# Kernel tuning notes

Measured on AMD Instinct MI355X. Metric: run time of the kernel, lower is better.

Reference implementation:

```python
import jax, jax.numpy as jnp
import numpy as np

EPS = 1e-5  # torch BatchNorm2d default eps


def _conv(x, w, b, pad):
    y = jax.lax.conv_general_dilated(
        x, w, window_strides=(1, 1), padding=[(pad, pad), (pad, pad)],
        dimension_numbers=('NCHW', 'OIHW', 'NCHW'))
    return y + b[None, :, None, None]


def _bn_train(x, gamma, beta):
    # training-mode BatchNorm2d: biased batch statistics over (N,H,W)
    m = jnp.mean(x, axis=(0, 2, 3), keepdims=True)
    v = jnp.var(x, axis=(0, 2, 3), keepdims=True)
    xn = (x - m) * jax.lax.rsqrt(v + EPS)
    return xn * gamma[None, :, None, None] + beta[None, :, None, None]


def _ncc(s, t):
    # Vectorized equivalent of the per-pixel double loop.
    # ncc[b,0,i,j] = mean(tt * ss / (tt_std * ss_std)) over (C,th,tw)
    #             = sum(tt * s_sub) / (N * tt_std * ss_std)   (since sum(tt)=0)
    b, c, sh, sw = s.shape
    th, tw = t.shape[2], t.shape[3]
    N = c * th * tw
    tt = t - jnp.mean(t, axis=(1, 2, 3), keepdims=True)
    # torch.std is unbiased (divides by N-1)
    tt_std = jnp.sqrt(jnp.sum(tt * tt, axis=(1, 2, 3), keepdims=True) / (N - 1))

    # cross[b] = valid correlation of s[b] with its own template tt[b]
    def per_sample(si, ti):
        return jax.lax.conv_general_dilated(
            si[None], ti[None], (1, 1), 'VALID',
            dimension_numbers=('NCHW', 'OIHW', 'NCHW'))[0]  # (1,h,w)

    cross = jax.vmap(per_sample)(s, tt)  # (b,1,h,w)

    # per-window mean/std of s via box-filter conv over all C channels jointly
    box = jnp.ones((1, c, th, tw), dtype=s.dtype)
    win_sum = jax.lax.conv_general_dilated(
        s, box, (1, 1), 'VALID', dimension_numbers=('NCHW', 'OIHW', 'NCHW'))
    win_sqsum = jax.lax.conv_general_dilated(
        s * s, box, (1, 1), 'VALID', dimension_numbers=('NCHW', 'OIHW', 'NCHW'))
    win_mean = win_sum / N
    ss_var = jnp.maximum(win_sqsum - N * win_mean * win_mean, 0.0) / (N - 1)
    ss_std = jnp.sqrt(ss_var)

    return cross / (N * tt_std * ss_std)  # (b,1,h,w)


def reference(s, t, w1, b1, g1, be1, w2, b2, g2, be2,
              w3, b3, g3, be3, w4, b4):
    s = _bn_train(_conv(s, w1, b1, pad=1), g1, be1)
    t = _bn_train(_conv(t, w2, b2, pad=1), g2, be2)
    ncc = _ncc(s, t)
    x = _bn_train(_conv(ncc, w3, b3, pad=0), g3, be3)
    x = jax.nn.relu(x)
    return _conv(x, w4, b4, pad=0)  # (b,2,h,w)


def setup_inputs() -> dict:
    key = jax.random.key(0)
    ks = jax.random.split(key, 12)
    C = 256
    inp = {
        's': jax.random.normal(ks[0], (16, C, 64, 64), jnp.float32),
        't': jax.random.normal(ks[1], (16, C, 16, 16), jnp.float32),
        'w1': jax.random.normal(ks[2], (C, C, 3, 3), jnp.float32) * 0.02,
        'b1': jax.random.normal(ks[3], (C,), jnp.float32) * 0.02,
        'g1': jnp.ones((C,), jnp.float32),
        'be1': jnp.zeros((C,), jnp.float32),
        'w2': jax.random.normal(ks[4], (C, C, 3, 3), jnp.float32) * 0.02,
        'b2': jax.random.normal(ks[5], (C,), jnp.float32) * 0.02,
        'g2': jnp.ones((C,), jnp.float32),
        'be2': jnp.zeros((C,), jnp.float32),
        'w3': jax.random.normal(ks[6], (1, 1, 1, 1), jnp.float32),
        'b3': jax.random.normal(ks[7], (1,), jnp.float32) * 0.02,
        'g3': jnp.ones((1,), jnp.float32),
        'be3': jnp.zeros((1,), jnp.float32),
        'w4': jax.random.normal(ks[8], (2, 1, 1, 1), jnp.float32),
        'b4': jax.random.normal(ks[9], (2,), jnp.float32) * 0.02,
    }
    return inp
```

## Files before the change

kernel.cpp:

```cpp
#include <hip/hip_runtime.h>
#include <hip/hip_bf16.h>

#define EPSV 1e-5f

constexpr int B_ = 16, C_ = 256;
constexpr int OHW_ = 49 * 49;
constexpr int NTOT = 256 * 16 * 16;
constexpr int GROUPS = 32, CPERG = 8;

typedef short bf16x8 __attribute__((ext_vector_type(8)));
typedef float f32x4 __attribute__((ext_vector_type(4)));

constexpr size_t OFF_S1 = 0;
constexpr size_t SZ_S1  = (size_t)16 * 256 * 4096;
constexpr size_t OFF_T2 = OFF_S1 + SZ_S1;
constexpr size_t SZ_T2  = (size_t)16 * 256 * 256;
constexpr size_t OFF_ST = OFF_T2 + SZ_T2;
constexpr size_t OFF_C  = OFF_ST + 2048;
constexpr size_t SPC_BYTES = (size_t)16 * 66 * 66 * 256 * 2;
constexpr size_t TPC_BYTES = (size_t)16 * 18 * 18 * 256 * 2;
constexpr size_t WR_BYTES  = (size_t)9 * 256 * 256 * 2;
constexpr size_t ZOFF  = 0;
constexpr size_t CPOFF = 131072;
constexpr size_t NCOFF = CPOFF + (size_t)GROUPS * 16 * OHW_;
constexpr size_t SATOFF = NCOFF + (size_t)16 * OHW_;

__device__ __forceinline__ void gload_lds16(const void* g, void* l) {
    __builtin_amdgcn_global_load_lds((const __attribute__((address_space(1))) unsigned int*)g,
                                     (__attribute__((address_space(3))) unsigned int*)l,
                                     16, 0, 0);
}

template<int W>
__global__ __launch_bounds__(256)
void pad_transpose(const float* __restrict__ in, __hip_bfloat16* __restrict__ outp)
{
    constexpr int PW = W + 2;
    __shared__ float tile[64][W + 1];
    int bid = blockIdx.x;
    int icg = bid & 3; bid >>= 2;
    int yp = bid % PW; bid /= PW;
    int b = bid;
    int ic0 = icg * 64;
    int tid = threadIdx.x;
    bool interior = (yp >= 1 && yp <= W);
    if (interior) {
        int y = yp - 1;
        for (int idx = tid; idx < 64 * W; idx += 256) {
            int i = idx / W, x = idx % W;
            tile[i][x] = in[(((size_t)(b * C_ + ic0 + i)) * W + y) * W + x];
        }
    }
    __syncthreads();
    for (int idx = tid; idx < PW * 16; idx += 256) {
        int xp = idx >> 4, i4 = idx & 15;
        ushort4 v = make_ushort4(0, 0, 0, 0);
        if (interior && xp >= 1 && xp <= W) {
            #pragma unroll
            for (int k = 0; k < 4; ++k) {
                __hip_bfloat16 h = __float2bfloat16(tile[i4 * 4 + k][xp - 1]);
                reinterpret_cast<unsigned short*>(&v)[k] = *reinterpret_cast<unsigned short*>(&h);
            }
        }
        *reinterpret_cast<ushort4*>(&outp[(((size_t)(b * PW) + yp) * PW + xp) * 256 + ic0 + i4 * 4]) = v;
    }
}

__global__ __launch_bounds__(256)
void weight_reorg(const float* __restrict__ w, __hip_bfloat16* __restrict__ wr)
{
    int idx = blockIdx.x * 256 + threadIdx.x;
    const float* src = w + (size_t)idx * 9;
    #pragma unroll
    for (int t = 0; t < 9; ++t)
        wr[(size_t)t * 65536 + idx] = __float2bfloat16(src[t]);
}

template<int W>
__global__ __launch_bounds__(256)
void conv_mfma(const __hip_bfloat16* __restrict__ SPc, const __hip_bfloat16* __restrict__ Wr,
               const float* __restrict__ bias, float* __restrict__ out,
               float* __restrict__ csum, float* __restrict__ csq)
{
    constexpr int PW = W + 2;
    constexpr int NPIX = W * W;
    constexpr int NT = NPIX / 128;
    __shared__ __hip_bfloat16 A_lds[128 * 32];
    __shared__ __hip_bfloat16 B_lds[128 * 32];

    int bid = blockIdx.x;
    int nt = bid % NT; bid /= NT;
    int mt = bid & 1;  bid >>= 1;
    int b  = bid;
    int tid = threadIdx.x;
    int lane = tid & 63;
    int wv = tid >> 6, wm = wv >> 1, wn = wv & 1;
    int oc0 = mt * 128, p0 = nt * 128;

    f32x4 acc[4][4];
    #pragma unroll
    for (int i = 0; i < 4; ++i)
        #pragma unroll
        for (int j = 0; j < 4; ++j)
            #pragma unroll
            for (int r = 0; r < 4; ++r) acc[i][j][r] = 0.f;

    const bf16x8* Af = reinterpret_cast<const bf16x8*>(A_lds);
    const bf16x8* Bf = reinterpret_cast<const bf16x8*>(B_lds);
    int colb = lane >> 4;
    int rA = lane & 15;

    for (int kc = 0; kc < 72; ++kc) {
        int tap = kc >> 3, icc = kc & 7;
        int ic0 = icc * 32;
        int dy = tap / 3, dx = tap - dy * 3;
        __syncthreads();
        #pragma unroll
        for (int it = 0; it < 2; ++it) {
            int sIdx = tid + it * 256;
            int row = sIdx >> 2, seg = sIdx & 3;
            const __hip_bfloat16* srcA =
                Wr + ((size_t)(tap * 256 + oc0 + row)) * 256 + ic0 + seg * 8;
            gload_lds16(srcA, &A_lds[sIdx * 8]);
            int p = p0 + row;
            int y = p / W, x = p % W;
            const __hip_bfloat16* srcB =
                SPc + (((size_t)(b * PW + y + dy)) * PW + x + dx) * 256 + ic0 + seg * 8;
            gload_lds16(srcB, &B_lds[sIdx * 8]);
        }
        asm volatile("s_waitcnt vmcnt(0)" ::: "memory");
        __syncthreads();

        bf16x8 a[4], bb[4];
        #pragma unroll
        for (int mi = 0; mi < 4; ++mi)
            a[mi] = Af[(wm * 64 + mi * 16 + rA) * 4 + colb];
        #pragma unroll
        for (int ni = 0; ni < 4; ++ni)
            bb[ni] = Bf[(wn * 64 + ni * 16 + rA) * 4 + colb];
        #pragma unroll
        for (int mi = 0; mi < 4; ++mi)
            #pragma unroll
            for (int ni = 0; ni < 4; ++ni)
                acc[mi][ni] = __builtin_amdgcn_mfma_f32_16x16x32_bf16(
                    a[mi], bb[ni], acc[mi][ni], 0, 0, 0);
    }

    #pragma unroll
    for (int mi = 0; mi < 4; ++mi) {
        int ocb = oc0 + wm * 64 + mi * 16 + (lane >> 4) * 4;
        #pragma unroll
        for (int r = 0; r < 4; ++r) {
            int oc = ocb + r;
            float bv = bias[oc];
            float* orow = out + ((size_t)(b * C_ + oc)) * NPIX;
            float s_oc = 0.f, q_oc = 0.f;
            #pragma unroll
            for (int ni = 0; ni < 4; ++ni) {
                int px = p0 + wn * 64 + ni * 16 + (lane & 15);
                float v = acc[mi][ni][r] + bv;
                orow[px] = v;
                s_oc += v; q_oc += v * v;
            }
            #pragma unroll
            for (int m_ = 1; m_ < 16; m_ <<= 1) {
                s_oc += __shfl_xor(s_oc, m_);
                q_oc += __shfl_xor(q_oc, m_);
            }
            if ((lane & 15) == 0) {
                atomicAdd(&csum[oc], s_oc);
                atomicAdd(&csq[oc], q_oc);
            }
        }
    }
}

__device__ inline void blk_reduce2(float& a, float& q, int tid) {
    #pragma unroll
    for (int off = 32; off > 0; off >>= 1) {
        a += __shfl_down(a, off);
        q += __shfl_down(q, off);
    }
    __shared__ float ra[4], rq[4];
    if ((tid & 63) == 0) { ra[tid >> 6] = a; rq[tid >> 6] = q; }
    __syncthreads();
    if (tid == 0) { a = ra[0] + ra[1] + ra[2] + ra[3]; q = rq[0] + rq[1] + rq[2] + rq[3]; }
}

__global__ __launch_bounds__(256)
void bn_norm(float* __restrict__ x, const float* __restrict__ csum,
             const float* __restrict__ csq, const float* __restrict__ g,
             const float* __restrict__ be, int HW, int total4, float inv_cnt)
{
    int i = blockIdx.x * 256 + threadIdx.x;
    if (i >= total4) return;
    int c = ((i * 4) / HW) % C_;
    float m = csum[c] * inv_cnt;
    float v = csq[c] * inv_cnt - m * m;
    float sc = rsqrtf(v + EPSV) * g[c];
    float sh = be[c] - m * sc;
    float4 val = reinterpret_cast<float4*>(x)[i];
    val.x = val.x * sc + sh;
    val.y = val.y * sc + sh;
    val.z = val.z * sc + sh;
    val.w = val.w * sc + sh;
    reinterpret_cast<float4*>(x)[i] = val;
}

__global__ __launch_bounds__(256)
void zplane_kernel(const float* __restrict__ s1, const float* __restrict__ csum,
                   const float* __restrict__ csq, const float* __restrict__ g1,
                   const float* __restrict__ be1, float* __restrict__ z)
{
    __shared__ float SC[256], SH[256];
    int tid = threadIdx.x;
    {
        float m = csum[tid] * (1.f / 65536.f);
        float v = csq[tid] * (1.f / 65536.f) - m * m;
        float sc = rsqrtf(v + EPSV) * g1[tid];
        SC[tid] = sc; SH[tid] = be1[tid] - m * sc;
    }
    __syncthreads();
    int i = blockIdx.x * 256 + tid;
    int b = i >> 12, p = i & 4095;
    const float* base = s1 + (size_t)b * (C_ * 4096) + p;
    float s = 0.f, q = 0.f;
    for (int c = 0; c < C_; ++c) {
        float val = base[(size_t)c * 4096] * SC[c] + SH[c];
        s += val; q += val * val;
    }
    z[i] = s; z[65536 + i] = q;
}

__global__ __launch_bounds__(256)
void sat_kernel(const float* __restrict__ zin, float* __restrict__ sat)
{
    __shared__ float t[65][66];
    int pl = blockIdx.x;
    int tid = threadIdx.x;
    const float* src = zin + (size_t)pl * 4096;
    for (int idx = tid; idx < 4096; idx += 256) {
        int y = idx >> 6, x = idx & 63;
        t[y + 1][x + 1] = src[idx];
    }
    for (int idx = tid; idx < 65; idx += 256) { t[0][idx] = 0.f; t[idx][0] = 0.f; }
    __syncthreads();
    if (tid < 64) {
        float run = 0.f;
        for (int x = 1; x <= 64; ++x) { run += t[tid + 1][x]; t[tid + 1][x] = run; }
    }
    __syncthreads();
    if (tid < 64) {
        float run = 0.f;
        for (int y = 1; y <= 64; ++y) { run += t[y][tid + 1]; t[y][tid + 1] = run; }
    }
    __syncthreads();
    float* dst = sat + (size_t)pl * 4225;
    for (int idx = tid; idx < 4225; idx += 256) {
        int r = idx / 65, c = idx % 65;
        dst[idx] = t[r][c];
    }
}

__global__ __launch_bounds__(256)
void tstat_kernel(const float* __restrict__ t2, float* __restrict__ tmean, float* __restrict__ ttstd)
{
    int b = blockIdx.x, tid = threadIdx.x;
    const float* p = t2 + (size_t)b * NTOT;
    float s = 0.f, q = 0.f;
    for (int i = tid; i < NTOT; i += 256) { float v = p[i]; s += v; q += v * v; }
    blk_reduce2(s, q, tid);
    if (tid == 0) {
        float m = s / (float)NTOT;
        tmean[b] = m;
        ttstd[b] = sqrtf(fmaxf(q - (float)NTOT * m * m, 0.f) / (float)(NTOT - 1));
    }
}

__global__ __launch_bounds__(256, 2)
void cross_v3(const float* __restrict__ s1, const float* __restrict__ t2,
              const float* __restrict__ csum, const float* __restrict__ csq,
              const float* __restrict__ g1, const float* __restrict__ be1,
              float* __restrict__ cpart)
{
    __shared__ float4 spl4[1024];
    __shared__ float tpl[256];
    __shared__ float red[4][64][49];

    int g = blockIdx.x & (GROUPS - 1);
    int b = blockIdx.x / GROUPS;
    int tid = threadIdx.x;
    int phase = tid >> 6;
    int lane = tid & 63;
    int i = lane;
    int i_ld = i < 49 ? i : 48;

    float acc[49];
    #pragma unroll
    for (int j = 0; j < 49; ++j) acc[j] = 0.f;

    #pragma unroll 1
    for (int cc = 0; cc < CPERG; ++cc) {
        int c = g * CPERG + cc;
        float m = csum[c] * (1.f / 65536.f);
        float v = csq[c] * (1.f / 65536.f) - m * m;
        float sc = rsqrtf(v + EPSV) * g1[c];
        float sh = be1[c] - m * sc;
        __syncthreads();
        const float4* sp4 = reinterpret_cast<const float4*>(s1 + ((size_t)(b * C_ + c)) * 4096);
        #pragma unroll
        for (int k = 0; k < 4; ++k) {
            int gidx = tid + k * 256;
            float4 val = sp4[gidx];
            val.x = val.x * sc + sh; val.y = val.y * sc + sh;
            val.z = val.z * sc + sh; val.w = val.w * sc + sh;
            int row = gidx >> 4, jg = gidx & 15;
            spl4[row * 16 + (jg ^ (row & 7))] = val;
        }
        tpl[tid] = t2[((size_t)(b * C_ + c)) * 256 + tid];
        __syncthreads();
        #pragma unroll 1
        for (int tyl = 0; tyl < 4; ++tyl) {
            int ty = phase * 4 + tyl;
            int row = i_ld + ty;
            float r_[64];
            #pragma unroll
            for (int jg = 0; jg < 16; ++jg) {
                float4 v4 = spl4[row * 16 + (jg ^ (row & 7))];
                r_[jg * 4 + 0] = v4.x; r_[jg * 4 + 1] = v4.y;
                r_[jg * 4 + 2] = v4.z; r_[jg * 4 + 3] = v4.w;
            }
            float tt[16];
            const float4* tp4 = reinterpret_cast<const float4*>(&tpl[ty * 16]);
            #pragma unroll
            for (int k = 0; k < 4; ++k) {
                float4 tv = tp4[k];
                tt[k * 4 + 0] = tv.x; tt[k * 4 + 1] = tv.y;
                tt[k * 4 + 2] = tv.z; tt[k * 4 + 3] = tv.w;
            }
            #pragma unroll
            for (int tx = 0; tx < 16; ++tx)
                #pragma unroll
                for (int j = 0; j < 49; ++j)
                    acc[j] += tt[tx] * r_[j + tx];
        }
    }
    __syncthreads();
    if (i < 49) {
        #pragma unroll
        for (int j = 0; j < 49; ++j) red[phase][i][j] = acc[j];
    }
    __syncthreads();
    float* dst = cpart + ((size_t)(g * B_ + b)) * OHW_;
    for (int e = tid; e < OHW_; e += 256) {
        int ii = e / 49, jj = e - ii * 49;
        dst[e] = red[0][ii][jj] + red[1][ii][jj] + red[2][ii][jj] + red[3][ii][jj];
    }
}

__global__ __launch_bounds__(256)
void ncc_kernel(const float* __restrict__ cpart, const float* __restrict__ sat,
                const float* __restrict__ tmean, const float* __restrict__ ttstd,
                float* __restrict__ ncc, float* __restrict__ s3)
{
    int idx = blockIdx.x * 256 + threadIdx.x;
    float val = 0.f;
    if (idx < B_ * OHW_) {
        int b = idx / OHW_, r = idx - b * OHW_;
        int i = r / 49, j = r - i * 49;
        float cr = 0.f;
        #pragma unroll 4
        for (int g = 0; g < GROUPS; ++g) cr += cpart[((size_t)(g * B_ + b)) * OHW_ + r];
        const float* sz = sat + (size_t)b * 4225;
        const float* sq = sat + (size_t)(16 + b) * 4225;
        int a00 = i * 65 + j, a01 = i * 65 + j + 16;
        int a10 = (i + 16) * 65 + j, a11 = (i + 16) * 65 + j + 16;
        float wsum = sz[a11] - sz[a01] - sz[a10] + sz[a00];
        float wq   = sq[a11] - sq[a01] - sq[a10] + sq[a00];
        float crosst = cr - tmean[b] * wsum;
        float ssvar = fmaxf(wq - wsum * wsum * (1.f / 65536.f), 0.f) * (1.f / 65535.f);
        float ssstd = sqrtf(ssvar);
        val = crosst / (65536.f * ttstd[b] * ssstd);
        ncc[idx] = val;
    }
    float s = val, q = val * val;
    blk_reduce2(s, q, threadIdx.x);
    if (threadIdx.x == 0) { atomicAdd(&s3[0], s); atomicAdd(&s3[1], q); }
}

__global__ __launch_bounds__(256)
void final_kernel(const float* __restrict__ ncc, const float* __restrict__ s3,
                  const float* __restrict__ w3, const float* __restrict__ b3,
                  const float* __restrict__ g3, const float* __restrict__ be3,
                  const float* __restrict__ w4, const float* __restrict__ b4,
                  float* __restrict__ out)
{
    int idx = blockIdx.x * 256 + threadIdx.x;
    if (idx >= B_ * OHW_) return;
    constexpr float M = (float)(B_ * OHW_);
    float mn = s3[0] / M;
    float vn = s3[1] / M - mn * mn;
    float W3 = w3[0], B3 = b3[0];
    float my = W3 * mn + B3;
    float vy = W3 * W3 * vn;
    float sc = rsqrtf(vy + EPSV) * g3[0];
    float y = (W3 * ncc[idx] + B3 - my) * sc + be3[0];
    float h = fmaxf(y, 0.f);
    int b = idx / OHW_, r = idx - b * OHW_;
    out[((size_t)(b * 2 + 0)) * OHW_ + r] = h * w4[0] + b4[0];
    out[((size_t)(b * 2 + 1)) * OHW_ + r] = h * w4[1] + b4[1];
}

extern "C" void kernel_launch(void* const* d_in, const int* in_sizes, int n_in,
                              void* d_out, int out_size, void* d_ws, size_t ws_size,
                              hipStream_t stream)
{
    const float* s   = (const float*)d_in[0];
    const float* t   = (const float*)d_in[1];
    const float* w1  = (const float*)d_in[2];
    const float* b1  = (const float*)d_in[3];
    const float* g1  = (const float*)d_in[4];
    const float* be1 = (const float*)d_in[5];
    const float* w2  = (const float*)d_in[6];
    const float* b2  = (const float*)d_in[7];
    const float* g2  = (const float*)d_in[8];
    const float* be2 = (const float*)d_in[9];
    const float* w3  = (const float*)d_in[10];
    const float* b3  = (const float*)d_in[11];
    const float* g3  = (const float*)d_in[12];
    const float* be3 = (const float*)d_in[13];
    const float* w4  = (const float*)d_in[14];
    const float* b4  = (const float*)d_in[15];

    float* ws = (float*)d_ws;
    float* S1 = ws + OFF_S1;
    float* T2 = ws + OFF_T2;
    float* ST = ws + OFF_ST;
    float* CHS1 = ST + 0;
    float* CHQ1 = ST + 256;
    float* CHS2 = ST + 512;
    float* CHQ2 = ST + 768;
    float* S3   = ST + 1024;
    float* TM   = ST + 1040;
    float* TSD  = ST + 1056;

    char* Cb = (char*)(ws + OFF_C);
    __hip_bfloat16* SPc = (__hip_bfloat16*)Cb;
    __hip_bfloat16* TPc = (__hip_bfloat16*)(Cb + SPC_BYTES);
    __hip_bfloat16* Wr1 = (__hip_bfloat16*)(Cb + SPC_BYTES + TPC_BYTES);
    __hip_bfloat16* Wr2 = (__hip_bfloat16*)(Cb + SPC_BYTES + TPC_BYTES + WR_BYTES);
    float* Cf = (float*)Cb;
    float* Z   = Cf + ZOFF;
    float* CP  = Cf + CPOFF;
    float* NC  = Cf + NCOFF;
    float* SAT = Cf + SATOFF;

    hipMemsetAsync(ST, 0, 1026 * sizeof(float), stream);

    pad_transpose<64><<<dim3(16 * 66 * 4), dim3(256), 0, stream>>>(s, SPc);
    pad_transpose<16><<<dim3(16 * 18 * 4), dim3(256), 0, stream>>>(t, TPc);
    weight_reorg<<<dim3(256), dim3(256), 0, stream>>>(w1, Wr1);
    weight_reorg<<<dim3(256), dim3(256), 0, stream>>>(w2, Wr2);

    conv_mfma<64><<<dim3(16 * 2 * 32), dim3(256), 0, stream>>>(SPc, Wr1, b1, S1, CHS1, CHQ1);
    conv_mfma<16><<<dim3(16 * 2 * 2),  dim3(256), 0, stream>>>(TPc, Wr2, b2, T2, CHS2, CHQ2);

    bn_norm<<<dim3(1024), dim3(256), 0, stream>>>(T2, CHS2, CHQ2, g2, be2, 256, 262144, 1.f / 4096.f);
    tstat_kernel<<<dim3(16), dim3(256), 0, stream>>>(T2, TM, TSD);

    zplane_kernel<<<dim3(256), dim3(256), 0, stream>>>(S1, CHS1, CHQ1, g1, be1, Z);
    sat_kernel<<<dim3(32), dim3(256), 0, stream>>>(Z, SAT);

    cross_v3<<<dim3(16 * GROUPS), dim3(256), 0, stream>>>(S1, T2, CHS1, CHQ1, g1, be1, CP);
    ncc_kernel<<<dim3(151), dim3(256), 0, stream>>>(CP, SAT, TM, TSD, NC, S3);
    final_kernel<<<dim3(151), dim3(256), 0, stream>>>(NC, S3, w3, b3, g3, be3, w4, b4, (float*)d_out);
}
```

Measured before the change: 488.6 us.

## Retile conv to 256x256 double-buffered MFMA and fold z-plane stats into cross

Activations and weights move to a 64-channel-blocked layout with XOR-swizzled LDS. The conv kernel now uses 512-thread blocks computing 256 output channels by 256 pixels, with double-buffered LDS staging, a K step of 64, wave priority hints and a block remap for the big conv. Separately, the per-pixel channel sum and sum-of-squares pass is removed: cross_v3 accumulates them while normalising, and writes them through atomics into a buffer zeroed by a memset. The aim is more data reuse and overlap in the conv and one fewer full read of S1, at the cost of more LDS, more registers and many atomics.

New measurement: 600.6 us. 22.9% more time.

```diff
diff --git a/kernel.cpp b/kernel.cpp
--- a/kernel.cpp
+++ b/kernel.cpp
@@ -17,9 +17,9 @@
 constexpr size_t SZ_T2  = (size_t)16 * 256 * 256;
 constexpr size_t OFF_ST = OFF_T2 + SZ_T2;
 constexpr size_t OFF_C  = OFF_ST + 2048;
-constexpr size_t SPC_BYTES = (size_t)16 * 66 * 66 * 256 * 2;
-constexpr size_t TPC_BYTES = (size_t)16 * 18 * 18 * 256 * 2;
-constexpr size_t WR_BYTES  = (size_t)9 * 256 * 256 * 2;
+constexpr size_t SPC_BYTES = (size_t)16 * 4 * 66 * 66 * 64 * 2;
+constexpr size_t TPC_BYTES = (size_t)16 * 4 * 18 * 18 * 64 * 2;
+constexpr size_t WR_BYTES  = (size_t)9 * 4 * 256 * 64 * 2;
 constexpr size_t ZOFF  = 0;
 constexpr size_t CPOFF = 131072;
 constexpr size_t NCOFF = CPOFF + (size_t)GROUPS * 16 * OHW_;
@@ -33,7 +33,7 @@
 
 template<int W>
 __global__ __launch_bounds__(256)
-void pad_transpose(const float* __restrict__ in, __hip_bfloat16* __restrict__ outp)
+void pad_transpose2(const float* __restrict__ in, __hip_bfloat16* __restrict__ outp)
 {
     constexpr int PW = W + 2;
     __shared__ float tile[64][W + 1];
@@ -52,6 +52,7 @@
         }
     }
     __syncthreads();
+    __hip_bfloat16* obase = outp + (((size_t)(b * 4 + icg) * PW + yp) * PW) * 64;
     for (int idx = tid; idx < PW * 16; idx += 256) {
         int xp = idx >> 4, i4 = idx & 15;
         ushort4 v = make_ushort4(0, 0, 0, 0);
@@ -62,102 +63,127 @@
                 reinterpret_cast<unsigned short*>(&v)[k] = *reinterpret_cast<unsigned short*>(&h);
             }
         }
-        *reinterpret_cast<ushort4*>(&outp[(((size_t)(b * PW) + yp) * PW + xp) * 256 + ic0 + i4 * 4]) = v;
-    }
-}
-
-__global__ __launch_bounds__(256)
-void weight_reorg(const float* __restrict__ w, __hip_bfloat16* __restrict__ wr)
+        *reinterpret_cast<ushort4*>(&obase[(size_t)xp * 64 + i4 * 4]) = v;
+    }
+}
+
+__global__ __launch_bounds__(256)
+void weight_reorg2(const float* __restrict__ w, __hip_bfloat16* __restrict__ wr)
 {
     int idx = blockIdx.x * 256 + threadIdx.x;
+    int oc = idx >> 8, ic = idx & 255;
+    int icc = ic >> 6, icl = ic & 63;
     const float* src = w + (size_t)idx * 9;
     #pragma unroll
     for (int t = 0; t < 9; ++t)
-        wr[(size_t)t * 65536 + idx] = __float2bfloat16(src[t]);
+        wr[(((size_t)(t * 4 + icc)) * 256 + oc) * 64 + icl] = __float2bfloat16(src[t]);
 }
 
 template<int W>
-__global__ __launch_bounds__(256)
-void conv_mfma(const __hip_bfloat16* __restrict__ SPc, const __hip_bfloat16* __restrict__ Wr,
-               const float* __restrict__ bias, float* __restrict__ out,
-               float* __restrict__ csum, float* __restrict__ csq)
+__global__ __launch_bounds__(512, 2)
+void conv_mfma2(const __hip_bfloat16* __restrict__ SPc, const __hip_bfloat16* __restrict__ Wr,
+                const float* __restrict__ bias, float* __restrict__ out,
+                float* __restrict__ csum, float* __restrict__ csq)
 {
     constexpr int PW = W + 2;
     constexpr int NPIX = W * W;
-    constexpr int NT = NPIX / 128;
-    __shared__ __hip_bfloat16 A_lds[128 * 32];
-    __shared__ __hip_bfloat16 B_lds[128 * 32];
+    constexpr int NT = NPIX / 256;
+    constexpr int RPT = 256 / W;
+    constexpr int NK = 36;
+
+    __shared__ __attribute__((aligned(16))) __hip_bfloat16 A_lds[2][256 * 64];
+    __shared__ __attribute__((aligned(16))) __hip_bfloat16 B_lds[2][256 * 64];
 
     int bid = blockIdx.x;
-    int nt = bid % NT; bid /= NT;
-    int mt = bid & 1;  bid >>= 1;
-    int b  = bid;
+    int logical = (W == 64) ? ((bid & 7) * 32 + (bid >> 3)) : bid;
+    int nt = logical % NT;
+    int b  = logical / NT;
     int tid = threadIdx.x;
     int lane = tid & 63;
-    int wv = tid >> 6, wm = wv >> 1, wn = wv & 1;
-    int oc0 = mt * 128, p0 = nt * 128;
-
-    f32x4 acc[4][4];
-    #pragma unroll
-    for (int i = 0; i < 4; ++i)
+    int wv = tid >> 6;
+    int wm = wv >> 2, wn = wv & 3;
+    int rA = lane & 15, colb = lane >> 4;
+
+    f32x4 acc[8][4];
+    #pragma unroll
+    for (int i = 0; i < 8; ++i)
         #pragma unroll
         for (int j = 0; j < 4; ++j)
             #pragma unroll
             for (int r = 0; r < 4; ++r) acc[i][j][r] = 0.f;
 
-    const bf16x8* Af = reinterpret_cast<const bf16x8*>(A_lds);
-    const bf16x8* Bf = reinterpret_cast<const bf16x8*>(B_lds);
-    int colb = lane >> 4;
-    int rA = lane & 15;
-
-    for (int kc = 0; kc < 72; ++kc) {
-        int tap = kc >> 3, icc = kc & 7;
-        int ic0 = icc * 32;
+    int pxs = tid >> 3;
+    int gp  = tid & 7;
+    int row0 = nt * RPT;
+
+    auto STAGE = [&](int buf, int kc) {
+        int tap = kc >> 2, icc = kc & 3;
         int dy = tap / 3, dx = tap - dy * 3;
+        const __hip_bfloat16* wsrc = Wr + (size_t)kc * (256 * 64);
+        const __hip_bfloat16* bsrc = SPc + (size_t)(b * 4 + icc) * (PW * PW * 64);
+        #pragma unroll
+        for (int r = 0; r < 4; ++r) {
+            int oc = r * 64 + pxs;
+            int ga = gp ^ (oc & 7);
+            gload_lds16(wsrc + (size_t)oc * 64 + ga * 8, &A_lds[buf][r * 4096 + tid * 8]);
+            int px = r * 64 + pxs;
+            int prow = px / W, pxx = px % W;
+            int gb = gp ^ (px & 7);
+            gload_lds16(bsrc + ((size_t)((row0 + prow + dy) * PW) + pxx + dx) * 64 + gb * 8,
+                        &B_lds[buf][r * 4096 + tid * 8]);
+        }
+    };
+
+    STAGE(0, 0);
+    __syncthreads();
+
+    for (int t = 0; t < NK; ++t) {
+        int buf = t & 1;
+        if (t + 1 < NK) STAGE(buf ^ 1, t + 1);
+
+        const bf16x8* Af = reinterpret_cast<const bf16x8*>(A_lds[buf]);
+        const bf16x8* Bf = reinterpret_cast<const bf16x8*>(B_lds[buf]);
+        #pragma unroll
+        for (int ks = 0; ks < 2; ++ks) {
+            bf16x8 a[8];
+            #pragma unroll
+            for (int mi = 0; mi < 8; ++mi) {
+                int row = wm * 128 + mi * 16 + rA;
+                a[mi] = Af[row * 8 + ((ks * 4 + colb) ^ (row & 7))];
+            }
+            #pragma unroll
+            for (int nh = 0; nh < 2; ++nh) {
+                bf16x8 bb[2];
+                #pragma unroll
+                for (int nj = 0; nj < 2; ++nj) {
+                    int row = wn * 64 + (nh * 2 + nj) * 16 + rA;
+                    bb[nj] = Bf[row * 8 + ((ks * 4 + colb) ^ (row & 7))];
+                }
+                __builtin_amdgcn_s_setprio(1);
+                #pragma unroll
+                for (int mi = 0; mi < 8; ++mi)
+                    #pragma unroll
+                    for (int nj = 0; nj < 2; ++nj)
+                        acc[mi][nh * 2 + nj] = __builtin_amdgcn_mfma_f32_16x16x32_bf16(
+                            a[mi], bb[nj], acc[mi][nh * 2 + nj], 0, 0, 0);
+                __builtin_amdgcn_s_setprio(0);
+            }
+        }
         __syncthreads();
-        #pragma unroll
-        for (int it = 0; it < 2; ++it) {
-            int sIdx = tid + it * 256;
-            int row = sIdx >> 2, seg = sIdx & 3;
-            const __hip_bfloat16* srcA =
-                Wr + ((size_t)(tap * 256 + oc0 + row)) * 256 + ic0 + seg * 8;
-            gload_lds16(srcA, &A_lds[sIdx * 8]);
-            int p = p0 + row;
-            int y = p / W, x = p % W;
-            const __hip_bfloat16* srcB =
-                SPc + (((size_t)(b * PW + y + dy)) * PW + x + dx) * 256 + ic0 + seg * 8;
-            gload_lds16(srcB, &B_lds[sIdx * 8]);
-        }
-        asm volatile("s_waitcnt vmcnt(0)" ::: "memory");
-        __syncthreads();
-
-        bf16x8 a[4], bb[4];
-        #pragma unroll
-        for (int mi = 0; mi < 4; ++mi)
-            a[mi] = Af[(wm * 64 + mi * 16 + rA) * 4 + colb];
-        #pragma unroll
-        for (int ni = 0; ni < 4; ++ni)
-            bb[ni] = Bf[(wn * 64 + ni * 16 + rA) * 4 + colb];
-        #pragma unroll
-        for (int mi = 0; mi < 4; ++mi)
-            #pragma unroll
-            for (int ni = 0; ni < 4; ++ni)
-                acc[mi][ni] = __builtin_amdgcn_mfma_f32_16x16x32_bf16(
-                    a[mi], bb[ni], acc[mi][ni], 0, 0, 0);
-    }
-
-    #pragma unroll
-    for (int mi = 0; mi < 4; ++mi) {
-        int ocb = oc0 + wm * 64 + mi * 16 + (lane >> 4) * 4;
+    }
+
+    #pragma unroll
+    for (int mi = 0; mi < 8; ++mi) {
+        int ocb = wm * 128 + mi * 16 + colb * 4;
         #pragma unroll
         for (int r = 0; r < 4; ++r) {
             int oc = ocb + r;
             float bv = bias[oc];
-            float* orow = out + ((size_t)(b * C_ + oc)) * NPIX;
+            float* orow = out + ((size_t)(b * C_ + oc)) * NPIX + nt * 256;
             float s_oc = 0.f, q_oc = 0.f;
             #pragma unroll
             for (int ni = 0; ni < 4; ++ni) {
-                int px = p0 + wn * 64 + ni * 16 + (lane & 15);
+                int px = wn * 64 + ni * 16 + rA;
                 float v = acc[mi][ni][r] + bv;
                 orow[px] = v;
                 s_oc += v; q_oc += v * v;
@@ -167,7 +193,7 @@
                 s_oc += __shfl_xor(s_oc, m_);
                 q_oc += __shfl_xor(q_oc, m_);
             }
-            if ((lane & 15) == 0) {
+            if (rA == 0) {
                 atomicAdd(&csum[oc], s_oc);
                 atomicAdd(&csq[oc], q_oc);
             }
@@ -208,31 +234,6 @@
 }
 
 __global__ __launch_bounds__(256)
-void zplane_kernel(const float* __restrict__ s1, const float* __restrict__ csum,
-                   const float* __restrict__ csq, const float* __restrict__ g1,
-                   const float* __restrict__ be1, float* __restrict__ z)
-{
-    __shared__ float SC[256], SH[256];
-    int tid = threadIdx.x;
-    {
-        float m = csum[tid] * (1.f / 65536.f);
-        float v = csq[tid] * (1.f / 65536.f) - m * m;
-        float sc = rsqrtf(v + EPSV) * g1[tid];
-        SC[tid] = sc; SH[tid] = be1[tid] - m * sc;
-    }
-    __syncthreads();
-    int i = blockIdx.x * 256 + tid;
-    int b = i >> 12, p = i & 4095;
-    const float* base = s1 + (size_t)b * (C_ * 4096) + p;
-    float s = 0.f, q = 0.f;
-    for (int c = 0; c < C_; ++c) {
-        float val = base[(size_t)c * 4096] * SC[c] + SH[c];
-        s += val; q += val * val;
-    }
-    z[i] = s; z[65536 + i] = q;
-}
-
-__global__ __launch_bounds__(256)
 void sat_kernel(const float* __restrict__ zin, float* __restrict__ sat)
 {
     __shared__ float t[65][66];
@@ -281,7 +282,7 @@
 void cross_v3(const float* __restrict__ s1, const float* __restrict__ t2,
               const float* __restrict__ csum, const float* __restrict__ csq,
               const float* __restrict__ g1, const float* __restrict__ be1,
-              float* __restrict__ cpart)
+              float* __restrict__ cpart, float* __restrict__ z)
 {
     __shared__ float4 spl4[1024];
     __shared__ float tpl[256];
@@ -298,6 +299,12 @@
     float acc[49];
     #pragma unroll
     for (int j = 0; j < 49; ++j) acc[j] = 0.f;
+    float4 zs[4], zq[4];
+    #pragma unroll
+    for (int k = 0; k < 4; ++k) {
+        zs[k] = make_float4(0.f, 0.f, 0.f, 0.f);
+        zq[k] = make_float4(0.f, 0.f, 0.f, 0.f);
+    }
 
     #pragma unroll 1
     for (int cc = 0; cc < CPERG; ++cc) {
@@ -314,6 +321,9 @@
             float4 val = sp4[gidx];
             val.x = val.x * sc + sh; val.y = val.y * sc + sh;
             val.z = val.z * sc + sh; val.w = val.w * sc + sh;
+            zs[k].x += val.x; zs[k].y += val.y; zs[k].z += val.z; zs[k].w += val.w;
+            zq[k].x += val.x * val.x; zq[k].y += val.y * val.y;
+            zq[k].z += val.z * val.z; zq[k].w += val.w * val.w;
             int row = gidx >> 4, jg = gidx & 15;
             spl4[row * 16 + (jg ^ (row & 7))] = val;
         }
@@ -344,6 +354,16 @@
                 for (int j = 0; j < 49; ++j)
                     acc[j] += tt[tx] * r_[j + tx];
         }
+    }
+    #pragma unroll
+    for (int k = 0; k < 4; ++k) {
+        int pxb = (tid + k * 256) * 4;
+        float* zb  = z + (size_t)b * 4096 + pxb;
+        float* z2b = z + 65536 + (size_t)b * 4096 + pxb;
+        atomicAdd(&zb[0], zs[k].x);  atomicAdd(&zb[1], zs[k].y);
+        atomicAdd(&zb[2], zs[k].z);  atomicAdd(&zb[3], zs[k].w);
+        atomicAdd(&z2b[0], zq[k].x); atomicAdd(&z2b[1], zq[k].y);
+        atomicAdd(&z2b[2], zq[k].z); atomicAdd(&z2b[3], zq[k].w);
     }
     __syncthreads();
     if (i < 49) {
@@ -457,21 +477,21 @@
 
     hipMemsetAsync(ST, 0, 1026 * sizeof(float), stream);
 
-    pad_transpose<64><<<dim3(16 * 66 * 4), dim3(256), 0, stream>>>(s, SPc);
-    pad_transpose<16><<<dim3(16 * 18 * 4), dim3(256), 0, stream>>>(t, TPc);
-    weight_reorg<<<dim3(256), dim3(256), 0, stream>>>(w1, Wr1);
-    weight_reorg<<<dim3(256), dim3(256), 0, stream>>>(w2, Wr2);
-
-    conv_mfma<64><<<dim3(16 * 2 * 32), dim3(256), 0, stream>>>(SPc, Wr1, b1, S1, CHS1, CHQ1);
-    conv_mfma<16><<<dim3(16 * 2 * 2),  dim3(256), 0, stream>>>(TPc, Wr2, b2, T2, CHS2, CHQ2);
+    pad_transpose2<64><<<dim3(16 * 66 * 4), dim3(256), 0, stream>>>(s, SPc);
+    pad_transpose2<16><<<dim3(16 * 18 * 4), dim3(256), 0, stream>>>(t, TPc);
+    weight_reorg2<<<dim3(256), dim3(256), 0, stream>>>(w1, Wr1);
+    weight_reorg2<<<dim3(256), dim3(256), 0, stream>>>(w2, Wr2);
+
+    conv_mfma2<64><<<dim3(256), dim3(512), 0, stream>>>(SPc, Wr1, b1, S1, CHS1, CHQ1);
+    conv_mfma2<16><<<dim3(16),  dim3(512), 0, stream>>>(TPc, Wr2, b2, T2, CHS2, CHQ2);
+
+    hipMemsetAsync(Z, 0, 2 * 65536 * sizeof(float), stream);
 
     bn_norm<<<dim3(1024), dim3(256), 0, stream>>>(T2, CHS2, CHQ2, g2, be2, 256, 262144, 1.f / 4096.f);
     tstat_kernel<<<dim3(16), dim3(256), 0, stream>>>(T2, TM, TSD);
 
-    zplane_kernel<<<dim3(256), dim3(256), 0, stream>>>(S1, CHS1, CHQ1, g1, be1, Z);
+    cross_v3<<<dim3(16 * GROUPS), dim3(256), 0, stream>>>(S1, T2, CHS1, CHQ1, g1, be1, CP, Z);
     sat_kernel<<<dim3(32), dim3(256), 0, stream>>>(Z, SAT);
-
-    cross_v3<<<dim3(16 * GROUPS), dim3(256), 0, stream>>>(S1, T2, CHS1, CHQ1, g1, be1, CP);
     ncc_kernel<<<dim3(151), dim3(256), 0, stream>>>(CP, SAT, TM, TSD, NC, S3);
     final_kernel<<<dim3(151), dim3(256), 0, stream>>>(NC, S3, w3, b3, g3, be3, w4, b4, (float*)d_out);
 }
```
